# Performance work log

Hardware: AMD Instinct MI355X
Metric: run time of the kernel (lower is better)

The kernel has to match this reference:

```python
import jax, jax.numpy as jnp
import numpy as np

B, C, H, W = 4, 96, 56, 56
K0, K1, DIL, HID = 5, 7, 3, 4  # HID: ConvMlp(dim, expansion, drop) => hidden_features = int(mlp_ratio) = 4 (repo quirk)
EPS = 1e-5


def _conv(x, w, b, pad, dil=1, groups=1):
    y = jax.lax.conv_general_dilated(x, w, (1, 1), [(pad, pad), (pad, pad)],
                                     rhs_dilation=(dil, dil),
                                     dimension_numbers=('NCHW', 'OIHW', 'NCHW'),
                                     feature_group_count=groups)
    return y + b[None, :, None, None]


def _conv1x1(x, w, b):
    return jnp.einsum('bchw,oc->bohw', x, w) + b[None, :, None, None]


def _ln(x, g, b):
    # LayerNormProxy: LayerNorm over channel dim of NCHW
    mu = jnp.mean(x, axis=1, keepdims=True)
    v = jnp.var(x, axis=1, keepdims=True)
    return (x - mu) * jax.lax.rsqrt(v + EPS) * g[None, :, None, None] + b[None, :, None, None]


def _gelu(x):
    return jax.nn.gelu(x, approximate=False)  # torch nn.GELU default = exact erf


def _deform_dw(x, ow, ob, dw, db, k, dil, pad):
    # DeformConv2d wrapper: offsets from a same-geometry conv, then depthwise deformable conv.
    Bx, Cx, Hx, Wx = x.shape
    P = k * k
    off = _conv(x, ow, ob, pad, dil).reshape(Bx, P, 2, Hx, Wx)  # [B,P,(y,x),H,W]
    ky = (jnp.repeat(jnp.arange(k), k) * dil - pad).astype(x.dtype)  # row-major kernel grid
    kx = (jnp.tile(jnp.arange(k), k) * dil - pad).astype(x.dtype)
    py = jnp.arange(Hx, dtype=x.dtype)[None, None, :, None] + ky[None, :, None, None] + off[:, :, 0]
    px = jnp.arange(Wx, dtype=x.dtype)[None, None, None, :] + kx[None, :, None, None] + off[:, :, 1]
    y0 = jnp.floor(py)
    x0 = jnp.floor(px)
    wy = py - y0
    wx = px - x0
    xf = x.reshape(Bx, Cx, Hx * Wx)

    def corner(yi, xi):
        valid = (yi >= 0) & (yi < Hx) & (xi >= 0) & (xi < Wx)
        idx = (jnp.clip(yi, 0, Hx - 1).astype(jnp.int32) * Wx
               + jnp.clip(xi, 0, Wx - 1).astype(jnp.int32)).reshape(Bx, -1)
        g = jax.vmap(lambda a, i: jnp.take(a, i, axis=1))(xf, idx).reshape(Bx, Cx, P, Hx, Wx)
        return g * valid[:, None].astype(x.dtype)

    v = (corner(y0, x0) * ((1 - wy) * (1 - wx))[:, None]
         + corner(y0, x0 + 1) * ((1 - wy) * wx)[:, None]
         + corner(y0 + 1, x0) * (wy * (1 - wx))[:, None]
         + corner(y0 + 1, x0 + 1) * (wy * wx)[:, None])  # [B,C,P,H,W]
    return jnp.einsum('bcphw,cp->bchw', v, dw) + db[None, :, None, None]


def setup_inputs() -> dict:
    key = jax.random.key(0)
    ks = iter(jax.random.split(key, 32))

    def rn(shape, s=1.0):
        return jax.random.normal(next(ks), shape, jnp.float32) * s

    f32 = jnp.float32
    return {
        'x': rn((B, C, H, W)),
        'g1n': jnp.ones((C,), f32), 'b1n': jnp.zeros((C,), f32),
        'p1w': rn((C, C), 1 / np.sqrt(C)), 'p1b': jnp.zeros((C,), f32),
        'o0w': rn((2 * K0 * K0, C, K0, K0), 0.05 / np.sqrt(C * K0 * K0)), 'o0b': jnp.zeros((2 * K0 * K0,), f32),
        'd0w': rn((C, K0 * K0), 1 / np.sqrt(K0 * K0)), 'd0b': jnp.zeros((C,), f32),
        'o1w': rn((2 * K1 * K1, C, K1, K1), 0.05 / np.sqrt(C * K1 * K1)), 'o1b': jnp.zeros((2 * K1 * K1,), f32),
        'd1w': rn((C, K1 * K1), 1 / np.sqrt(K1 * K1)), 'd1b': jnp.zeros((C,), f32),
        'c1w': rn((C, C), 1 / np.sqrt(C)), 'c1b': jnp.zeros((C,), f32),
        'p2w': rn((C, C), 1 / np.sqrt(C)), 'p2b': jnp.zeros((C,), f32),
        'ls1': jnp.full((C,), 0.01, f32),
        'g2n': jnp.ones((C,), f32), 'b2n': jnp.zeros((C,), f32),
        'f1w': rn((HID, C), 1 / np.sqrt(C)), 'f1b': jnp.zeros((HID,), f32),
        'dww': rn((HID, 1, 3, 3), 1 / 3.0), 'dwb': jnp.zeros((HID,), f32),
        'f2w': rn((C, HID), 1 / np.sqrt(HID)), 'f2b': jnp.zeros((C,), f32),
        'ls2': jnp.full((C,), 0.01, f32),
    }


def reference(x, g1n, b1n, p1w, p1b, o0w, o0b, d0w, d0b, o1w, o1b, d1w, d1b,
              c1w, c1b, p2w, p2b, ls1, g2n, b2n, f1w, f1b, dww, dwb, f2w, f2b, ls2):
    # attention branch
    y = _ln(x, g1n, b1n)
    shortcut = y
    y = _gelu(_conv1x1(y, p1w, p1b))
    u = y
    a = _deform_dw(y, o0w, o0b, d0w, d0b, K0, 1, K0 // 2)
    a = _deform_dw(a, o1w, o1b, d1w, d1b, K1, DIL, (K1 // 2) * DIL)
    a = _conv1x1(a, c1w, c1b)
    y = _conv1x1(u * a, p2w, p2b) + shortcut
    y = ls1[None, :, None, None] * y
    x = x + y
    # MLP branch (note: norm2 is applied to the branch output y, as in the source)
    z = _ln(y, g2n, b2n)
    z = _conv1x1(z, f1w, f1b)
    z = _gelu(_conv(z, dww, dwb, 1, 1, HID))
    z = _conv1x1(z, f2w, f2b)
    x = x + ls2[None, :, None, None] * z
    return x
```

## Files before the change

### kernel.cpp

```cpp
#include <hip/hip_runtime.h>
#include <math.h>

namespace {

constexpr int Bc = 4, Cc = 96, Hc = 56, Wc = 56;
constexpr int HWc = Hc * Wc;
constexpr int Nc  = Bc * HWc;
constexpr float EPSc = 1e-5f;

typedef __attribute__((ext_vector_type(8))) short bf16x8;
typedef __attribute__((ext_vector_type(4))) float f32x4;

__device__ __forceinline__ unsigned short f2bf(float f) {
  union { float f; unsigned u; } x; x.f = f;
  unsigned r = x.u + 0x7fffu + ((x.u >> 16) & 1u);
  return (unsigned short)(r >> 16);
}
__device__ __forceinline__ float bf2f(unsigned short u) {
  union { unsigned u; float f; } x; x.u = (unsigned)u << 16; return x.f;
}
__device__ __forceinline__ float gelu_exact(float x) {
  return 0.5f * x * (1.0f + erff(x * 0.7071067811865475f));
}

__global__ __launch_bounds__(256) void k_ln(const float* __restrict__ x,
                                            const float* __restrict__ g,
                                            const float* __restrict__ b,
                                            unsigned short* __restrict__ outN) {
  int pos = blockIdx.x * 256 + threadIdx.x;
  int bb = pos / HWc, hw = pos % HWc;
  const float* xb = x + (size_t)bb * Cc * HWc + hw;
  float s = 0.f, s2 = 0.f;
  for (int c = 0; c < Cc; ++c) { float v = xb[c * HWc]; s += v; s2 += v * v; }
  float mu  = s * (1.f / Cc);
  float var = fmaxf(s2 * (1.f / Cc) - mu * mu, 0.f);
  float rs  = rsqrtf(var + EPSc);
  unsigned short* ob = outN + (size_t)pos * Cc;
  for (int q = 0; q < 12; ++q) {
    unsigned short t8[8];
#pragma unroll
    for (int j = 0; j < 8; ++j) {
      int c = q * 8 + j;
      t8[j] = f2bf((xb[c * HWc] - mu) * rs * g[c] + b[c]);
    }
    *reinterpret_cast<bf16x8*>(ob + q * 8) = *reinterpret_cast<const bf16x8*>(t8);
  }
}

template <int K_, int MTILES, int P>
__global__ __launch_bounds__(256) void k_pack_w(const float* __restrict__ wsrc,
                                                unsigned short* __restrict__ wpk) {
  constexpr int TOTAL = K_ * K_ * 3 * MTILES * 512;
  int idx = blockIdx.x * 256 + threadIdx.x;
  if (idx >= TOTAL) return;
  int j    = idx & 7;
  int lane = (idx >> 3) & 63;
  int t    = idx >> 9;
  int mt   = t % MTILES;
  int step = t / MTILES;
  int o = mt * 16 + (lane & 15);
  int k = step * 32 + ((lane >> 4) & 3) * 8 + j;
  int p = k / Cc, c = k % Cc;
  float v = 0.f;
  if (o < P) v = wsrc[(((size_t)o * Cc + c) * K_ + p / K_) * K_ + (p % K_)];
  wpk[idx] = f2bf(v);
}

__global__ __launch_bounds__(256) void k_pack_dwt(const float* __restrict__ dwsrc,
                                                  float* __restrict__ dwt, int KK) {
  int idx = blockIdx.x * 256 + threadIdx.x;
  if (idx >= KK * Cc) return;
  int p = idx / Cc, c = idx % Cc;
  dwt[idx] = dwsrc[c * KK + p];
}

template <int GELU, int PADP, int WP>
__global__ __launch_bounds__(256) void k_pwg(const unsigned short* __restrict__ inN,
                                             const unsigned short* __restrict__ wpk,
                                             const float* __restrict__ bq,
                                             unsigned short* __restrict__ outPad) {
  int lane = threadIdx.x & 63;
  int wv = threadIdx.x >> 6;
  int ng = wv & 1, mg = wv >> 1;
  int n = blockIdx.x * 32 + ng * 16 + (lane & 15);
  int ko = ((lane >> 4) & 3) * 8;
  const unsigned short* ib = inN + (size_t)n * Cc + ko;
  const unsigned short* wl = wpk + (size_t)lane * 8;
  f32x4 acc[3];
#pragma unroll
  for (int m = 0; m < 3; ++m) acc[m] = (f32x4){0.f, 0.f, 0.f, 0.f};
#pragma unroll
  for (int ks = 0; ks < 3; ++ks) {
    bf16x8 bf = *reinterpret_cast<const bf16x8*>(ib + ks * 32);
#pragma unroll
    for (int m = 0; m < 3; ++m) {
      bf16x8 af = *reinterpret_cast<const bf16x8*>(wl + (size_t)(ks * 6 + mg * 3 + m) * 512);
      acc[m] = __builtin_amdgcn_mfma_f32_16x16x32_bf16(af, bf, acc[m], 0, 0, 0);
    }
  }
  int bb = n / HWc, hw = n % HWc;
  int h = hw / Wc, w = hw % Wc;
  unsigned short* ob = outPad + (((size_t)bb * (Hc + 2 * PADP) + h + PADP) * WP + w + PADP) * Cc;
  int orow = ((lane >> 4) & 3) * 4;
#pragma unroll
  for (int m = 0; m < 3; ++m) {
    int o0 = (mg * 3 + m) * 16 + orow;
    float4 bv = *reinterpret_cast<const float4*>(bq + o0);
    unsigned short t4[4];
#pragma unroll
    for (int j = 0; j < 4; ++j) {
      float r = acc[m][j] + ((const float*)&bv)[j];
      if (GELU) r = gelu_exact(r);
      t4[j] = f2bf(r);
    }
    *reinterpret_cast<uint2*>(ob + o0) = *reinterpret_cast<const uint2*>(t4);
  }
}

template <int UPADP, int UWP>
__global__ __launch_bounds__(256) void k_comb(const unsigned short* __restrict__ uPad,
                                              const unsigned short* __restrict__ An,
                                              const unsigned short* __restrict__ wpk,
                                              const float* __restrict__ bq,
                                              const unsigned short* __restrict__ ylnN,
                                              const float* __restrict__ ls1q,
                                              const float* __restrict__ x,
                                              float* __restrict__ out,
                                              unsigned short* __restrict__ y2N) {
  int lane = threadIdx.x & 63;
  int wv = threadIdx.x >> 6;
  int ng = wv & 1, mg = wv >> 1;
  int n = blockIdx.x * 32 + ng * 16 + (lane & 15);
  int ko = ((lane >> 4) & 3) * 8;
  int bb = n / HWc, hw = n % HWc;
  int h = hw / Wc, w = hw % Wc;
  const unsigned short* ub = uPad + (((size_t)bb * (Hc + 2 * UPADP) + h + UPADP) * UWP + w + UPADP) * Cc + ko;
  const unsigned short* ab = An + (size_t)n * Cc + ko;
  const unsigned short* wl = wpk + (size_t)lane * 8;
  f32x4 acc[3];
#pragma unroll
  for (int m = 0; m < 3; ++m) acc[m] = (f32x4){0.f, 0.f, 0.f, 0.f};
#pragma unroll
  for (int ks = 0; ks < 3; ++ks) {
    bf16x8 uv = *reinterpret_cast<const bf16x8*>(ub + ks * 32);
    bf16x8 av = *reinterpret_cast<const bf16x8*>(ab + ks * 32);
    union { bf16x8 v; unsigned short s[8]; } uu, aa, gg;
    uu.v = uv; aa.v = av;
#pragma unroll
    for (int j = 0; j < 8; ++j) gg.s[j] = f2bf(bf2f(uu.s[j]) * bf2f(aa.s[j]));
#pragma unroll
    for (int m = 0; m < 3; ++m) {
      bf16x8 af = *reinterpret_cast<const bf16x8*>(wl + (size_t)(ks * 6 + mg * 3 + m) * 512);
      acc[m] = __builtin_amdgcn_mfma_f32_16x16x32_bf16(af, gg.v, acc[m], 0, 0, 0);
    }
  }
  int orow = ((lane >> 4) & 3) * 4;
  const float* xb = x + (size_t)bb * Cc * HWc + hw;
  float* ob = out + (size_t)bb * Cc * HWc + hw;
#pragma unroll
  for (int m = 0; m < 3; ++m) {
    int o0 = (mg * 3 + m) * 16 + orow;
    float4 bv = *reinterpret_cast<const float4*>(bq + o0);
    float4 lv = *reinterpret_cast<const float4*>(ls1q + o0);
    uint2 yl = *reinterpret_cast<const uint2*>(ylnN + (size_t)n * Cc + o0);
    unsigned short yl4[4];
    *reinterpret_cast<uint2*>(yl4) = yl;
    unsigned short t4[4];
#pragma unroll
    for (int j = 0; j < 4; ++j) {
      float t = acc[m][j] + ((const float*)&bv)[j] + bf2f(yl4[j]);
      float y2 = ((const float*)&lv)[j] * t;
      t4[j] = f2bf(y2);
      ob[(size_t)(o0 + j) * HWc] = xb[(size_t)(o0 + j) * HWc] + y2;
    }
    *reinterpret_cast<uint2*>(y2N + (size_t)n * Cc + o0) = *reinterpret_cast<const uint2*>(t4);
  }
}

template <int K_, int DIL_, int MTILES, int MT, int P, int PADP, int WP, int PSTR, int SPLIT>
__global__ __launch_bounds__(256) void k_conv_mfma(const unsigned short* __restrict__ inp,
                                                   const unsigned short* __restrict__ wpk,
                                                   const float* __restrict__ bq,
                                                   float* __restrict__ dstT) {
  constexpr int KK = K_ * K_;
  constexpr int KKbase = KK / SPLIT, KKrem = KK % SPLIT;
  constexpr int HP = Hc + 2 * PADP;
  constexpr int NBLK = Nc / 32;
  int lane = threadIdx.x & 63;
  int wv = threadIdx.x >> 6;
  int bid = blockIdx.x;
  int sp = blockIdx.y;
  int p0 = sp * KKbase + min(sp, KKrem);
  int pcnt = KKbase + (sp < KKrem ? 1 : 0);
  int ntile = (bid & 7) * (NBLK / 8) + (bid >> 3);
  int n0 = ntile * 32 + (lane & 15);
  int n1 = n0 + 16;
  int b0 = n0 / HWc, hw0 = n0 % HWc, h0 = hw0 / Wc, w0 = hw0 % Wc;
  int b1 = n1 / HWc, hw1 = n1 % HWc, h1 = hw1 / Wc, w1 = hw1 % Wc;
  int co = ((lane >> 4) & 3) * 8;
  const unsigned short* ib0 = inp + ((size_t)b0 * HP * WP + (size_t)h0 * WP + w0) * Cc + co;
  const unsigned short* ib1 = inp + ((size_t)b1 * HP * WP + (size_t)h1 * WP + w1) * Cc + co;
  const unsigned short* wl = wpk + (size_t)lane * 8;
  int mt0 = wv * MT;
  int mtc[MT];
#pragma unroll
  for (int i = 0; i < MT; ++i) mtc[i] = min(mt0 + i, MTILES - 1);

  f32x4 acc[MT][2];
#pragma unroll
  for (int i = 0; i < MT; ++i) {
    acc[i][0] = (f32x4){0.f, 0.f, 0.f, 0.f};
    acc[i][1] = (f32x4){0.f, 0.f, 0.f, 0.f};
  }

  bf16x8 Bb[3][2], Aa[MT][3];
  {
    size_t toff = (size_t)((p0 / K_) * DIL_ * WP + (p0 % K_) * DIL_) * Cc;
#pragma unroll
    for (int cc = 0; cc < 3; ++cc) {
      Bb[cc][0] = *reinterpret_cast<const bf16x8*>(ib0 + toff + cc * 32);
      Bb[cc][1] = *reinterpret_cast<const bf16x8*>(ib1 + toff + cc * 32);
#pragma unroll
      for (int i = 0; i < MT; ++i)
        Aa[i][cc] = *reinterpret_cast<const bf16x8*>(wl + ((size_t)(p0 * 3 + cc) * MTILES + mtc[i]) * 512);
    }
  }

#pragma unroll 2
  for (int pi = 0; pi < pcnt; ++pi) {
    int pn = p0 + ((pi + 1 < pcnt) ? pi + 1 : pi);
    size_t toff = (size_t)((pn / K_) * DIL_ * WP + (pn % K_) * DIL_) * Cc;
    const unsigned short* sp0 = ib0 + toff;
    const unsigned short* sp1 = ib1 + toff;
    bf16x8 Bn[3][2], An[MT][3];
#pragma unroll
    for (int cc = 0; cc < 3; ++cc) {
      Bn[cc][0] = *reinterpret_cast<const bf16x8*>(sp0 + cc * 32);
      Bn[cc][1] = *reinterpret_cast<const bf16x8*>(sp1 + cc * 32);
#pragma unroll
      for (int i = 0; i < MT; ++i)
        An[i][cc] = *reinterpret_cast<const bf16x8*>(wl + ((size_t)(pn * 3 + cc) * MTILES + mtc[i]) * 512);
    }
#pragma unroll
    for (int cc = 0; cc < 3; ++cc)
#pragma unroll
      for (int i = 0; i < MT; ++i) {
        acc[i][0] = __builtin_amdgcn_mfma_f32_16x16x32_bf16(Aa[i][cc], Bb[cc][0], acc[i][0], 0, 0, 0);
        acc[i][1] = __builtin_amdgcn_mfma_f32_16x16x32_bf16(Aa[i][cc], Bb[cc][1], acc[i][1], 0, 0, 0);
      }
#pragma unroll
    for (int cc = 0; cc < 3; ++cc) {
      Bb[cc][0] = Bn[cc][0];
      Bb[cc][1] = Bn[cc][1];
#pragma unroll
      for (int i = 0; i < MT; ++i) Aa[i][cc] = An[i][cc];
    }
  }

  float* dsp = dstT + (size_t)sp * Nc * PSTR;
  int orow = ((lane >> 4) & 3) * 4;
#pragma unroll
  for (int i = 0; i < MT; ++i) {
    int mt = mt0 + i;
    if (mt >= MTILES) break;
#pragma unroll
    for (int nt = 0; nt < 2; ++nt) {
      float4 st;
#pragma unroll
      for (int j = 0; j < 4; ++j) {
        int o = mt * 16 + orow + j;
        float bias = (sp == 0 && o < P) ? bq[o] : 0.f;
        ((float*)&st)[j] = acc[i][nt][j] + bias;
      }
      int n = nt ? n1 : n0;
      *reinterpret_cast<float4*>(dsp + (size_t)n * PSTR + mt * 16 + orow) = st;
    }
  }
}

template <int K_, int DIL_, int PAD_, int PSTR, int NSUM>
__global__ __launch_bounds__(256) void k_meta(const float* __restrict__ offT,
                                              uint4* __restrict__ meta) {
  constexpr int KK = K_ * K_;
  int idx = blockIdx.x * 256 + threadIdx.x;
  if (idx >= Nc * KK) return;
  int p = idx % KK, pos = idx / KK;
  int hw = pos % HWc;
  int h = hw / Wc, w = hw % Wc;
  const float* ob = offT + (size_t)pos * PSTR + 2 * p;
  float oy = ob[0], ox = ob[1];
#pragma unroll
  for (int q = 1; q < NSUM; ++q) {
    oy += ob[(size_t)q * Nc * PSTR];
    ox += ob[(size_t)q * Nc * PSTR + 1];
  }
  float py = (float)(h + (p / K_) * DIL_ - PAD_) + oy;
  float px = (float)(w + (p % K_) * DIL_ - PAD_) + ox;
  float y0f = floorf(py), x0f = floorf(px);
  float wy = py - y0f, wx = px - x0f;
  int y0 = (int)y0f, x0 = (int)x0f;
  int y1 = y0 + 1, x1 = x0 + 1;
  bool y0v = (unsigned)y0 < (unsigned)Hc, y1v = (unsigned)y1 < (unsigned)Hc;
  bool x0v = (unsigned)x0 < (unsigned)Wc, x1v = (unsigned)x1 < (unsigned)Wc;
  int y0c = min(max(y0, 0), Hc - 1), y1c = min(max(y1, 0), Hc - 1);
  int x0c = min(max(x0, 0), Wc - 1), x1c = min(max(x1, 0), Wc - 1);
  float w00 = (y0v && x0v) ? (1.f - wy) * (1.f - wx) : 0.f;
  float w01 = (y0v && x1v) ? (1.f - wy) * wx : 0.f;
  float w10 = (y1v && x0v) ? wy * (1.f - wx) : 0.f;
  float w11 = (y1v && x1v) ? wy * wx : 0.f;
  uint4 m;
  m.x = (unsigned)(y0c | (y1c << 6) | (x0c << 12) | (x1c << 18));
  m.y = 0;
  m.z = (unsigned)f2bf(w00) | ((unsigned)f2bf(w01) << 16);
  m.w = (unsigned)f2bf(w10) | ((unsigned)f2bf(w11) << 16);
  meta[idx] = m;
}

template <int K_, int IPADP, int IWP, int OPADP, int OWP>
__global__ __launch_bounds__(256) void k_deform3(const unsigned short* __restrict__ srcT,
                                                 const uint4* __restrict__ meta,
                                                 const float* __restrict__ dwt,
                                                 const float* __restrict__ dbq,
                                                 unsigned short* __restrict__ dstPad) {
  constexpr int KK = K_ * K_;
  constexpr int IHP = Hc + 2 * IPADP;
  __shared__ float sdwt[KK * Cc];
  for (int i = threadIdx.x; i < KK * Cc; i += 256) sdwt[i] = dwt[i];
  __syncthreads();

  int tid = blockIdx.x * 256 + threadIdx.x;
  int cg = tid % 24;
  int pos = tid / 24;
  int c = cg * 4;
  int bb = pos / HWc, hw = pos % HWc;
  int h = hw / Wc, w = hw % Wc;
  const unsigned short* sb = srcT + ((size_t)bb * IHP * IWP + IPADP * IWP + IPADP) * Cc + c;
  const uint4* mt = meta + (size_t)pos * KK;
  float ac0 = 0.f, ac1 = 0.f, ac2 = 0.f, ac3 = 0.f;

  constexpr int BT = 4;
  int p = 0;
  for (; p + BT <= KK; p += BT) {
    uint4 m[BT];
#pragma unroll
    for (int i = 0; i < BT; ++i) m[i] = mt[p + i];
    uint2 v[BT][4];
#pragma unroll
    for (int i = 0; i < BT; ++i) {
      unsigned ix = m[i].x;
      int y0 = (int)(ix & 63u), y1 = (int)((ix >> 6) & 63u);
      int x0 = (int)((ix >> 12) & 63u), x1 = (int)((ix >> 18) & 63u);
      const unsigned short* r0 = sb + (size_t)(y0 * IWP) * Cc;
      const unsigned short* r1 = sb + (size_t)(y1 * IWP) * Cc;
      v[i][0] = *reinterpret_cast<const uint2*>(r0 + x0 * Cc);
      v[i][1] = *reinterpret_cast<const uint2*>(r0 + x1 * Cc);
      v[i][2] = *reinterpret_cast<const uint2*>(r1 + x0 * Cc);
      v[i][3] = *reinterpret_cast<const uint2*>(r1 + x1 * Cc);
    }
#pragma unroll
    for (int i = 0; i < BT; ++i) {
      float w00 = bf2f((unsigned short)(m[i].z & 0xffffu));
      float w01 = bf2f((unsigned short)(m[i].z >> 16));
      float w10 = bf2f((unsigned short)(m[i].w & 0xffffu));
      float w11 = bf2f((unsigned short)(m[i].w >> 16));
      float4 d = *reinterpret_cast<const float4*>(&sdwt[(p + i) * Cc + c]);
#pragma unroll
      for (int j = 0; j < 2; ++j) {
        unsigned u00 = ((const unsigned*)&v[i][0])[j];
        unsigned u01 = ((const unsigned*)&v[i][1])[j];
        unsigned u10 = ((const unsigned*)&v[i][2])[j];
        unsigned u11 = ((const unsigned*)&v[i][3])[j];
        union { unsigned u; float f; } a0_, b0_, a1_, b1_, a2_, b2_, a3_, b3_;
        a0_.u = u00 << 16; b0_.u = u00 & 0xffff0000u;
        a1_.u = u01 << 16; b1_.u = u01 & 0xffff0000u;
        a2_.u = u10 << 16; b2_.u = u10 & 0xffff0000u;
        a3_.u = u11 << 16; b3_.u = u11 & 0xffff0000u;
        float lo = w00 * a0_.f + w01 * a1_.f + w10 * a2_.f + w11 * a3_.f;
        float hi = w00 * b0_.f + w01 * b1_.f + w10 * b2_.f + w11 * b3_.f;
        if (j == 0) { ac0 += lo * d.x; ac1 += hi * d.y; }
        else        { ac2 += lo * d.z; ac3 += hi * d.w; }
      }
    }
  }
  {
    uint4 m = mt[p];
    unsigned ix = m.x;
    int y0 = (int)(ix & 63u), y1 = (int)((ix >> 6) & 63u);
    int x0 = (int)((ix >> 12) & 63u), x1 = (int)((ix >> 18) & 63u);
    const unsigned short* r0 = sb + (size_t)(y0 * IWP) * Cc;
    const unsigned short* r1 = sb + (size_t)(y1 * IWP) * Cc;
    uint2 v0 = *reinterpret_cast<const uint2*>(r0 + x0 * Cc);
    uint2 v1 = *reinterpret_cast<const uint2*>(r0 + x1 * Cc);
    uint2 v2 = *reinterpret_cast<const uint2*>(r1 + x0 * Cc);
    uint2 v3 = *reinterpret_cast<const uint2*>(r1 + x1 * Cc);
    float w00 = bf2f((unsigned short)(m.z & 0xffffu));
    float w01 = bf2f((unsigned short)(m.z >> 16));
    float w10 = bf2f((unsigned short)(m.w & 0xffffu));
    float w11 = bf2f((unsigned short)(m.w >> 16));
    float4 d = *reinterpret_cast<const float4*>(&sdwt[p * Cc + c]);
#pragma unroll
    for (int j = 0; j < 2; ++j) {
      unsigned u00 = ((const unsigned*)&v0)[j];
      unsigned u01 = ((const unsigned*)&v1)[j];
      unsigned u10 = ((const unsigned*)&v2)[j];
      unsigned u11 = ((const unsigned*)&v3)[j];
      union { unsigned u; float f; } a0_, b0_, a1_, b1_, a2_, b2_, a3_, b3_;
      a0_.u = u00 << 16; b0_.u = u00 & 0xffff0000u;
      a1_.u = u01 << 16; b1_.u = u01 & 0xffff0000u;
      a2_.u = u10 << 16; b2_.u = u10 & 0xffff0000u;
      a3_.u = u11 << 16; b3_.u = u11 & 0xffff0000u;
      float lo = w00 * a0_.f + w01 * a1_.f + w10 * a2_.f + w11 * a3_.f;
      float hi = w00 * b0_.f + w01 * b1_.f + w10 * b2_.f + w11 * b3_.f;
      if (j == 0) { ac0 += lo * d.x; ac1 += hi * d.y; }
      else        { ac2 += lo * d.z; ac3 += hi * d.w; }
    }
  }

  unsigned short t4[4] = {f2bf(ac0 + dbq[c]), f2bf(ac1 + dbq[c + 1]),
                          f2bf(ac2 + dbq[c + 2]), f2bf(ac3 + dbq[c + 3])};
  unsigned short* tb = dstPad + (((size_t)bb * (Hc + 2 * OPADP) + h + OPADP) * OWP + w + OPADP) * Cc + c;
  *reinterpret_cast<uint2*>(tb) = *reinterpret_cast<const uint2*>(t4);
}

__global__ __launch_bounds__(256) void k_mlp1(const unsigned short* __restrict__ y2N,
                                              const float* __restrict__ g,
                                              const float* __restrict__ b,
                                              const float* __restrict__ f1wq,
                                              const float* __restrict__ f1bq,
                                              float* __restrict__ z4) {
  int pos = blockIdx.x * 256 + threadIdx.x;
  int bb = pos / HWc, hw = pos % HWc;
  const unsigned short* yb = y2N + (size_t)pos * Cc;
  float vv[96];
  float s = 0.f, s2 = 0.f;
#pragma unroll
  for (int q = 0; q < 12; ++q) {
    bf16x8 t = *reinterpret_cast<const bf16x8*>(yb + q * 8);
    union { bf16x8 v; unsigned short s[8]; } u; u.v = t;
#pragma unroll
    for (int j = 0; j < 8; ++j) {
      float f = bf2f(u.s[j]);
      vv[q * 8 + j] = f; s += f; s2 += f * f;
    }
  }
  float mu  = s * (1.f / Cc);
  float var = fmaxf(s2 * (1.f / Cc) - mu * mu, 0.f);
  float rs  = rsqrtf(var + EPSc);
  float a0 = 0.f, a1 = 0.f, a2 = 0.f, a3 = 0.f;
#pragma unroll
  for (int c = 0; c < 96; ++c) {
    float t = (vv[c] - mu) * rs * g[c] + b[c];
    a0 += t * f1wq[0 * Cc + c];
    a1 += t * f1wq[1 * Cc + c];
    a2 += t * f1wq[2 * Cc + c];
    a3 += t * f1wq[3 * Cc + c];
  }
  float* zb = z4 + (size_t)bb * 4 * HWc + hw;
  zb[0 * HWc] = a0 + f1bq[0];
  zb[1 * HWc] = a1 + f1bq[1];
  zb[2 * HWc] = a2 + f1bq[2];
  zb[3 * HWc] = a3 + f1bq[3];
}

__global__ __launch_bounds__(256) void k_mlp_dw(const float* __restrict__ z4,
                                                const float* __restrict__ dwwq,
                                                const float* __restrict__ dwbq,
                                                float* __restrict__ z4b) {
  int tid = blockIdx.x * 256 + threadIdx.x;
  int hw = tid % HWc;
  int bj = tid / HWc;
  int j = bj % 4;
  int h = hw / Wc, w = hw % Wc;
  const float* zb = z4 + (size_t)bj * HWc;
  float s = 0.f;
#pragma unroll
  for (int ky = 0; ky < 3; ++ky) {
    int y = h + ky - 1;
    if ((unsigned)y >= (unsigned)Hc) continue;
#pragma unroll
    for (int kx = 0; kx < 3; ++kx) {
      int x = w + kx - 1;
      if ((unsigned)x >= (unsigned)Wc) continue;
      s += zb[y * Wc + x] * dwwq[j * 9 + ky * 3 + kx];
    }
  }
  z4b[tid] = gelu_exact(s + dwbq[j]);
}

__global__ __launch_bounds__(256) void k_mlp2(const float* __restrict__ z4b,
                                              const float* __restrict__ f2wq,
                                              const float* __restrict__ f2bq,
                                              const float* __restrict__ ls2q,
                                              float* __restrict__ out) {
  int pos = blockIdx.x * 256 + threadIdx.x;
  int bb = pos / HWc, hw = pos % HWc;
  const float* zb = z4b + (size_t)bb * 4 * HWc + hw;
  float z0 = zb[0 * HWc], z1 = zb[1 * HWc], z2 = zb[2 * HWc], z3 = zb[3 * HWc];
  float* ob = out + (size_t)bb * Cc * HWc + hw;
  for (int o = 0; o < Cc; ++o) {
    float s = f2bq[o] + z0 * f2wq[o * 4 + 0] + z1 * f2wq[o * 4 + 1]
                      + z2 * f2wq[o * 4 + 2] + z3 * f2wq[o * 4 + 3];
    ob[o * HWc] += ls2q[o] * s;
  }
}

}

extern "C" void kernel_launch(void* const* d_in, const int* in_sizes, int n_in,
                              void* d_out, int out_size, void* d_ws, size_t ws_size,
                              hipStream_t stream) {
  (void)in_sizes; (void)n_in; (void)out_size; (void)ws_size;
  const float* x   = (const float*)d_in[0];
  const float* g1n = (const float*)d_in[1];
  const float* b1n = (const float*)d_in[2];
  const float* p1w = (const float*)d_in[3];
  const float* p1b = (const float*)d_in[4];
  const float* o0w = (const float*)d_in[5];
  const float* o0b = (const float*)d_in[6];
  const float* d0w = (const float*)d_in[7];
  const float* d0b = (const float*)d_in[8];
  const float* o1w = (const float*)d_in[9];
  const float* o1b = (const float*)d_in[10];
  const float* d1w = (const float*)d_in[11];
  const float* d1b = (const float*)d_in[12];
  const float* c1w = (const float*)d_in[13];
  const float* c1b = (const float*)d_in[14];
  const float* p2w = (const float*)d_in[15];
  const float* p2b = (const float*)d_in[16];
  const float* ls1 = (const float*)d_in[17];
  const float* g2n = (const float*)d_in[18];
  const float* b2n = (const float*)d_in[19];
  const float* f1w = (const float*)d_in[20];
  const float* f1b = (const float*)d_in[21];
  const float* dww = (const float*)d_in[22];
  const float* dwb = (const float*)d_in[23];
  const float* f2w = (const float*)d_in[24];
  const float* f2b = (const float*)d_in[25];
  const float* ls2 = (const float*)d_in[26];
  float* out = (float*)d_out;
  float* ws  = (float*)d_ws;

  float* off0t = ws;                                  size_t o_ = (size_t)2 * Nc * 64;
  float* off1t = ws + o_;                             o_ += (size_t)4 * Nc * 112;
  float* z4    = ws + o_;                             o_ += (size_t)Bc * 4 * HWc;
  float* z4b   = ws + o_;                             o_ += (size_t)Bc * 4 * HWc;
  float* dwt0  = ws + o_;                             o_ += 25 * Cc;
  float* dwt1  = ws + o_;                             o_ += 49 * Cc + 4;
  o_ = (o_ + 3) & ~(size_t)3;
  uint4* metaM0 = (uint4*)(ws + o_);                  o_ += (size_t)Nc * 25 * 4;
  uint4* metaM1 = (uint4*)(ws + o_);                  o_ += (size_t)Nc * 49 * 4;
  unsigned short* yln_n  = (unsigned short*)(ws + o_); o_ += (size_t)Nc * Cc / 2;
  unsigned short* a1_n   = (unsigned short*)(ws + o_); o_ += (size_t)Nc * Cc / 2;
  unsigned short* A_n    = (unsigned short*)(ws + o_); o_ += (size_t)Nc * Cc / 2;
  unsigned short* y2_n   = (unsigned short*)(ws + o_); o_ += (size_t)Nc * Cc / 2;
  unsigned short* u_pad  = (unsigned short*)(ws + o_); o_ += (size_t)Bc * 60 * 60 * Cc / 2;
  unsigned short* a0_pad = (unsigned short*)(ws + o_); o_ += (size_t)Bc * 74 * 74 * Cc / 2;
  unsigned short* wpk0   = (unsigned short*)(ws + o_); o_ += (size_t)25 * 3 * 4 * 512 / 2;
  unsigned short* wpk1   = (unsigned short*)(ws + o_); o_ += (size_t)49 * 3 * 7 * 512 / 2;
  unsigned short* wpkp1  = (unsigned short*)(ws + o_); o_ += (size_t)3 * 6 * 512 / 2;
  unsigned short* wpkc1  = (unsigned short*)(ws + o_); o_ += (size_t)3 * 6 * 512 / 2;
  unsigned short* wpkp2  = (unsigned short*)(ws + o_); o_ += (size_t)3 * 6 * 512 / 2;

  dim3 b256(256, 1, 1);

  hipMemsetAsync(u_pad, 0, (size_t)Bc * 60 * 60 * Cc * sizeof(unsigned short), stream);
  hipMemsetAsync(a0_pad, 0, (size_t)Bc * 74 * 74 * Cc * sizeof(unsigned short), stream);
  hipLaunchKernelGGL((k_pack_w<5, 4, 50>), dim3((25 * 3 * 4 * 512 + 255) / 256), b256, 0, stream, o0w, wpk0);
  hipLaunchKernelGGL((k_pack_w<7, 7, 98>), dim3((49 * 3 * 7 * 512 + 255) / 256), b256, 0, stream, o1w, wpk1);
  hipLaunchKernelGGL((k_pack_w<1, 6, 96>), dim3((3 * 6 * 512 + 255) / 256), b256, 0, stream, p1w, wpkp1);
  hipLaunchKernelGGL((k_pack_w<1, 6, 96>), dim3((3 * 6 * 512 + 255) / 256), b256, 0, stream, c1w, wpkc1);
  hipLaunchKernelGGL((k_pack_w<1, 6, 96>), dim3((3 * 6 * 512 + 255) / 256), b256, 0, stream, p2w, wpkp2);
  hipLaunchKernelGGL(k_pack_dwt, dim3((25 * Cc + 255) / 256), b256, 0, stream, d0w, dwt0, 25);
  hipLaunchKernelGGL(k_pack_dwt, dim3((49 * Cc + 255) / 256), b256, 0, stream, d1w, dwt1, 49);

  hipLaunchKernelGGL(k_ln, dim3(Nc / 256), b256, 0, stream, x, g1n, b1n, yln_n);
  hipLaunchKernelGGL((k_pwg<1, 2, 60>), dim3(Nc / 32), b256, 0, stream, yln_n, wpkp1, p1b, u_pad);
  hipLaunchKernelGGL((k_conv_mfma<5, 1, 4, 1, 50, 2, 60, 64, 2>), dim3(Nc / 32, 2), b256, 0, stream,
                     u_pad, wpk0, o0b, off0t);
  hipLaunchKernelGGL((k_meta<5, 1, 2, 64, 2>), dim3((Nc * 25 + 255) / 256), b256, 0, stream,
                     off0t, metaM0);
  hipLaunchKernelGGL((k_deform3<5, 2, 60, 9, 74>), dim3(Nc * 24 / 256), b256, 0, stream,
                     u_pad, metaM0, dwt0, d0b, a0_pad);
  hipLaunchKernelGGL((k_conv_mfma<7, 3, 7, 2, 98, 9, 74, 112, 4>), dim3(Nc / 32, 4), b256, 0, stream,
                     a0_pad, wpk1, o1b, off1t);
  hipLaunchKernelGGL((k_meta<7, 3, 9, 112, 4>), dim3((Nc * 49 + 255) / 256), b256, 0, stream,
                     off1t, metaM1);
  hipLaunchKernelGGL((k_deform3<7, 9, 74, 0, 56>), dim3(Nc * 24 / 256), b256, 0, stream,
                     a0_pad, metaM1, dwt1, d1b, a1_n);
  hipLaunchKernelGGL((k_pwg<0, 0, 56>), dim3(Nc / 32), b256, 0, stream, a1_n, wpkc1, c1b, A_n);
  hipLaunchKernelGGL((k_comb<2, 60>), dim3(Nc / 32), b256, 0, stream,
                     u_pad, A_n, wpkp2, p2b, yln_n, ls1, x, out, y2_n);
  hipLaunchKernelGGL(k_mlp1, dim3(Nc / 256), b256, 0, stream, y2_n, g2n, b2n, f1w, f1b, z4);
  hipLaunchKernelGGL(k_mlp_dw, dim3(Nc * 4 / 256), b256, 0, stream, z4, dww, dwb, z4b);
  hipLaunchKernelGGL(k_mlp2, dim3(Nc / 256), b256, 0, stream, z4b, f2w, f2b, ls2, out);
}
```

Before: 231.5 us.

## Give each wave all output tiles for its own 32 positions in offset convs

```diff
diff --git a/kernel.cpp b/kernel.cpp
--- a/kernel.cpp
+++ b/kernel.cpp
@@ -10,6 +10,7 @@
 
 typedef __attribute__((ext_vector_type(8))) short bf16x8;
 typedef __attribute__((ext_vector_type(4))) float f32x4;
+typedef __attribute__((ext_vector_type(4))) unsigned int u32x4;
 
 __device__ __forceinline__ unsigned short f2bf(float f) {
   union { float f; unsigned u; } x; x.f = f;
@@ -177,23 +178,20 @@
   }
 }
 
-template <int K_, int DIL_, int MTILES, int MT, int P, int PADP, int WP, int PSTR, int SPLIT>
+template <int K_, int DIL_, int MTILES, int P, int PADP, int WP, int PSTR, int SPLIT>
 __global__ __launch_bounds__(256) void k_conv_mfma(const unsigned short* __restrict__ inp,
                                                    const unsigned short* __restrict__ wpk,
                                                    const float* __restrict__ bq,
                                                    float* __restrict__ dstT) {
   constexpr int KK = K_ * K_;
-  constexpr int KKbase = KK / SPLIT, KKrem = KK % SPLIT;
+  constexpr int KKb = KK / SPLIT, KKr = KK % SPLIT;
   constexpr int HP = Hc + 2 * PADP;
-  constexpr int NBLK = Nc / 32;
   int lane = threadIdx.x & 63;
   int wv = threadIdx.x >> 6;
-  int bid = blockIdx.x;
   int sp = blockIdx.y;
-  int p0 = sp * KKbase + min(sp, KKrem);
-  int pcnt = KKbase + (sp < KKrem ? 1 : 0);
-  int ntile = (bid & 7) * (NBLK / 8) + (bid >> 3);
-  int n0 = ntile * 32 + (lane & 15);
+  int p0 = sp * KKb + min(sp, KKr);
+  int pcnt = KKb + (sp < KKr ? 1 : 0);
+  int n0 = blockIdx.x * 128 + wv * 32 + (lane & 15);
   int n1 = n0 + 16;
   int b0 = n0 / HWc, hw0 = n0 % HWc, h0 = hw0 / Wc, w0 = hw0 % Wc;
   int b1 = n1 / HWc, hw1 = n1 % HWc, h1 = hw1 / Wc, w1 = hw1 % Wc;
@@ -201,68 +199,39 @@
   const unsigned short* ib0 = inp + ((size_t)b0 * HP * WP + (size_t)h0 * WP + w0) * Cc + co;
   const unsigned short* ib1 = inp + ((size_t)b1 * HP * WP + (size_t)h1 * WP + w1) * Cc + co;
   const unsigned short* wl = wpk + (size_t)lane * 8;
-  int mt0 = wv * MT;
-  int mtc[MT];
-#pragma unroll
-  for (int i = 0; i < MT; ++i) mtc[i] = min(mt0 + i, MTILES - 1);
-
-  f32x4 acc[MT][2];
-#pragma unroll
-  for (int i = 0; i < MT; ++i) {
-    acc[i][0] = (f32x4){0.f, 0.f, 0.f, 0.f};
-    acc[i][1] = (f32x4){0.f, 0.f, 0.f, 0.f};
-  }
-
-  bf16x8 Bb[3][2], Aa[MT][3];
-  {
-    size_t toff = (size_t)((p0 / K_) * DIL_ * WP + (p0 % K_) * DIL_) * Cc;
+
+  f32x4 acc[MTILES][2];
+#pragma unroll
+  for (int mt = 0; mt < MTILES; ++mt) {
+    acc[mt][0] = (f32x4){0.f, 0.f, 0.f, 0.f};
+    acc[mt][1] = (f32x4){0.f, 0.f, 0.f, 0.f};
+  }
+
+  for (int pi = 0; pi < pcnt; ++pi) {
+    int p = p0 + pi;
+    size_t toff = (size_t)((p / K_) * DIL_ * WP + (p % K_) * DIL_) * Cc;
+    union { u32x4 u; bf16x8 v; } b0r[3], b1r[3];
 #pragma unroll
     for (int cc = 0; cc < 3; ++cc) {
-      Bb[cc][0] = *reinterpret_cast<const bf16x8*>(ib0 + toff + cc * 32);
-      Bb[cc][1] = *reinterpret_cast<const bf16x8*>(ib1 + toff + cc * 32);
-#pragma unroll
-      for (int i = 0; i < MT; ++i)
-        Aa[i][cc] = *reinterpret_cast<const bf16x8*>(wl + ((size_t)(p0 * 3 + cc) * MTILES + mtc[i]) * 512);
-    }
-  }
-
-#pragma unroll 2
-  for (int pi = 0; pi < pcnt; ++pi) {
-    int pn = p0 + ((pi + 1 < pcnt) ? pi + 1 : pi);
-    size_t toff = (size_t)((pn / K_) * DIL_ * WP + (pn % K_) * DIL_) * Cc;
-    const unsigned short* sp0 = ib0 + toff;
-    const unsigned short* sp1 = ib1 + toff;
-    bf16x8 Bn[3][2], An[MT][3];
+      b0r[cc].u = __builtin_nontemporal_load(reinterpret_cast<const u32x4*>(ib0 + toff + cc * 32));
+      b1r[cc].u = __builtin_nontemporal_load(reinterpret_cast<const u32x4*>(ib1 + toff + cc * 32));
+    }
 #pragma unroll
     for (int cc = 0; cc < 3; ++cc) {
-      Bn[cc][0] = *reinterpret_cast<const bf16x8*>(sp0 + cc * 32);
-      Bn[cc][1] = *reinterpret_cast<const bf16x8*>(sp1 + cc * 32);
-#pragma unroll
-      for (int i = 0; i < MT; ++i)
-        An[i][cc] = *reinterpret_cast<const bf16x8*>(wl + ((size_t)(pn * 3 + cc) * MTILES + mtc[i]) * 512);
-    }
-#pragma unroll
-    for (int cc = 0; cc < 3; ++cc)
-#pragma unroll
-      for (int i = 0; i < MT; ++i) {
-        acc[i][0] = __builtin_amdgcn_mfma_f32_16x16x32_bf16(Aa[i][cc], Bb[cc][0], acc[i][0], 0, 0, 0);
-        acc[i][1] = __builtin_amdgcn_mfma_f32_16x16x32_bf16(Aa[i][cc], Bb[cc][1], acc[i][1], 0, 0, 0);
+      const unsigned short* wa = wl + (size_t)(p * 3 + cc) * MTILES * 512;
+#pragma unroll
+      for (int mt = 0; mt < MTILES; ++mt) {
+        bf16x8 A = *reinterpret_cast<const bf16x8*>(wa + (size_t)mt * 512);
+        acc[mt][0] = __builtin_amdgcn_mfma_f32_16x16x32_bf16(A, b0r[cc].v, acc[mt][0], 0, 0, 0);
+        acc[mt][1] = __builtin_amdgcn_mfma_f32_16x16x32_bf16(A, b1r[cc].v, acc[mt][1], 0, 0, 0);
       }
-#pragma unroll
-    for (int cc = 0; cc < 3; ++cc) {
-      Bb[cc][0] = Bn[cc][0];
-      Bb[cc][1] = Bn[cc][1];
-#pragma unroll
-      for (int i = 0; i < MT; ++i) Aa[i][cc] = An[i][cc];
     }
   }
 
   float* dsp = dstT + (size_t)sp * Nc * PSTR;
   int orow = ((lane >> 4) & 3) * 4;
 #pragma unroll
-  for (int i = 0; i < MT; ++i) {
-    int mt = mt0 + i;
-    if (mt >= MTILES) break;
+  for (int mt = 0; mt < MTILES; ++mt) {
 #pragma unroll
     for (int nt = 0; nt < 2; ++nt) {
       float4 st;
@@ -270,7 +239,7 @@
       for (int j = 0; j < 4; ++j) {
         int o = mt * 16 + orow + j;
         float bias = (sp == 0 && o < P) ? bq[o] : 0.f;
-        ((float*)&st)[j] = acc[i][nt][j] + bias;
+        ((float*)&st)[j] = acc[mt][nt][j] + bias;
       }
       int n = nt ? n1 : n0;
       *reinterpret_cast<float4*>(dsp + (size_t)n * PSTR + mt * 16 + orow) = st;
@@ -575,13 +544,13 @@
 
   hipLaunchKernelGGL(k_ln, dim3(Nc / 256), b256, 0, stream, x, g1n, b1n, yln_n);
   hipLaunchKernelGGL((k_pwg<1, 2, 60>), dim3(Nc / 32), b256, 0, stream, yln_n, wpkp1, p1b, u_pad);
-  hipLaunchKernelGGL((k_conv_mfma<5, 1, 4, 1, 50, 2, 60, 64, 2>), dim3(Nc / 32, 2), b256, 0, stream,
+  hipLaunchKernelGGL((k_conv_mfma<5, 1, 4, 50, 2, 60, 64, 2>), dim3(Nc / 128, 2), b256, 0, stream,
                      u_pad, wpk0, o0b, off0t);
   hipLaunchKernelGGL((k_meta<5, 1, 2, 64, 2>), dim3((Nc * 25 + 255) / 256), b256, 0, stream,
                      off0t, metaM0);
   hipLaunchKernelGGL((k_deform3<5, 2, 60, 9, 74>), dim3(Nc * 24 / 256), b256, 0, stream,
                      u_pad, metaM0, dwt0, d0b, a0_pad);
-  hipLaunchKernelGGL((k_conv_mfma<7, 3, 7, 2, 98, 9, 74, 112, 4>), dim3(Nc / 32, 4), b256, 0, stream,
+  hipLaunchKernelGGL((k_conv_mfma<7, 3, 7, 98, 9, 74, 112, 4>), dim3(Nc / 128, 4), b256, 0, stream,
                      a0_pad, wpk1, o1b, off1t);
   hipLaunchKernelGGL((k_meta<7, 3, 9, 112, 4>), dim3((Nc * 49 + 255) / 256), b256, 0, stream,
                      off1t, metaM1);
```

Result: slower. 249.3 us (+7.7%).
